# Optimization experiments

Hardware: AMD Instinct MI355X
Metric: run time of the kernel (lower is better)

The kernel has to match this reference:

```python
import jax, jax.numpy as jnp
import numpy as np

B = 4096      # batch
F = 26        # num sparse features
L = 10        # pooling factor (multi-hot indices per feature)
V = 100000    # rows per embedding table
D = 128       # embedding dim (== dense_arch_layer_sizes[-1])
DENSE_IN = 13
DENSE_SIZES = [512, 256, 128]
OVER_SIZES = [1024, 1024, 512, 256, 1]
OVER_IN = D + (F * (F - 1)) // 2 + F  # 479


def _linear_params(key, dims, prefix):
    out = {}
    ks = jax.random.split(key, len(dims) - 1)
    for i in range(len(dims) - 1):
        fan_in = dims[i]
        out[f"{prefix}W{i}"] = jax.random.normal(ks[i], (dims[i], dims[i + 1]), jnp.float32) / np.sqrt(fan_in)
        out[f"{prefix}b{i}"] = jnp.zeros((dims[i + 1],), jnp.float32)
    return out


def setup_inputs() -> dict:
    key = jax.random.key(0)
    k0, k1, k2, k3, k4 = jax.random.split(key, 5)
    inp = {
        "dense_features": jax.random.normal(k0, (B, DENSE_IN), jnp.float32),
        "indices": jax.random.randint(k1, (B, F, L), 0, V, dtype=jnp.int64),
        "tables": jax.random.normal(k2, (F, V, D), jnp.float32) * 0.01,
    }
    inp.update(_linear_params(k3, [DENSE_IN] + DENSE_SIZES, "d"))
    inp.update(_linear_params(k4, [OVER_IN] + OVER_SIZES, "o"))
    return inp


def _dlrm_forward(dense_features, indices, tables,
                  dW0, db0, dW1, db1, dW2, db2,
                  oW0, ob0, oW1, ob1, oW2, ob2, oW3, ob3, oW4, ob4):
    b = dense_features.shape[0]
    # DenseArch: MLP with relu on every layer
    x = dense_features
    for W, bb in ((dW0, db0), (dW1, db1), (dW2, db2)):
        x = jax.nn.relu(x @ W + bb)
    embedded_dense = x  # [B, D]

    # SparseArch: pooled (sum) embedding lookup per feature -> [B, F, D]
    flat_tables = tables.reshape(F * V, D)
    offs = jnp.arange(F, dtype=indices.dtype) * V
    flat_idx = (indices + offs[None, :, None]).reshape(-1)
    gathered = jnp.take(flat_tables, flat_idx, axis=0).reshape(b, F, L, D)
    embedded_sparse = gathered.sum(axis=2)  # [B, F, D]

    # InteractionArch: bmm + upper-triangular gather
    z = jnp.concatenate([embedded_dense[:, None, :], embedded_sparse], axis=1)  # [B, F+1, D]
    inter = jnp.einsum("bnd,bmd->bnm", z, z)  # [B, F+1, F+1]
    iu0, iu1 = np.triu_indices(F + 1, k=1)
    inter_flat = inter[:, iu0, iu1]  # [B, C(F+1,2)]
    feats = jnp.concatenate([embedded_dense, inter_flat], axis=1)  # [B, OVER_IN]

    # OverArch: relu MLP on layer_sizes[:-1], then plain final Linear
    y = feats
    for W, bb in ((oW0, ob0), (oW1, ob1), (oW2, ob2), (oW3, ob3)):
        y = jax.nn.relu(y @ W + bb)
    logits = y @ oW4 + ob4  # [B, 1]
    return logits


def reference(dense_features, indices, tables,
              dW0, db0, dW1, db1, dW2, db2,
              oW0, ob0, oW1, ob1, oW2, ob2, oW3, ob3, oW4, ob4):
    return _dlrm_forward(dense_features, indices, tables,
                         dW0, db0, dW1, db1, dW2, db2,
                         oW0, ob0, oW1, ob1, oW2, ob2, oW3, ob3, oW4, ob4)
```

## Files before the change

### kernel.cpp

```cpp
#include <hip/hip_runtime.h>

#define B_ 4096
#define F_ 26
#define L_ 10
#define V_ 100000
#define D_ 128

typedef __attribute__((ext_vector_type(8))) short short8;
typedef __attribute__((ext_vector_type(4))) float f32x4;

__device__ inline unsigned pack_split(float f) {
    union { float f; unsigned u; } a; a.f = f;
    unsigned r = (a.u + 0x7FFFu + ((a.u >> 16) & 1u)) >> 16;
    union { unsigned u; float f; } hf; hf.u = r << 16;
    float rem = f - hf.f;
    union { float f; unsigned u; } b; b.f = rem;
    unsigned r2 = (b.u + 0x7FFFu + ((b.u >> 16) & 1u)) >> 16;
    return (r << 16) | (r2 & 0xFFFFu);
}
__device__ inline float unpack_f(unsigned u) {
    union { unsigned u; float f; } h; h.u = u & 0xFFFF0000u;
    union { unsigned u; float f; } l; l.u = u << 16;
    return h.f + l.f;
}

__device__ void prep_tile(const float* __restrict__ W, unsigned* __restrict__ Wt,
                          int K, int N, int Kp, int local)
{
    __shared__ float tile[32][33];
    const int t = threadIdx.x;
    const int tx = t & 31, ty = t >> 5;
    const int nbt = N >> 5;
    const int nb = (local % nbt) << 5, kb = (local / nbt) << 5;
    #pragma unroll
    for (int i = 0; i < 4; ++i) {
        int k = kb + ty + i * 8;
        tile[ty + i * 8][tx] = (k < K) ? W[(size_t)k * N + nb + tx] : 0.f;
    }
    __syncthreads();
    #pragma unroll
    for (int i = 0; i < 4; ++i) {
        int nl = ty + i * 8;
        Wt[(size_t)(nb + nl) * Kp + kb + tx] = pack_split(tile[tx][nl]);
    }
}

__global__ __launch_bounds__(256) void prep_all(
    const float* dW0, const float* dW1, const float* dW2,
    const float* oW0, const float* oW1, const float* oW2, const float* oW3,
    unsigned* dWt0, unsigned* dWt1, unsigned* dWt2,
    unsigned* oWt0, unsigned* oWt1, unsigned* oWt2, unsigned* oWt3,
    const float* dense, unsigned* densep)
{
    const int bid = blockIdx.x;
    if      (bid < 16)   prep_tile(dW0, dWt0, 13,   512,  32,   bid);
    else if (bid < 144)  prep_tile(dW1, dWt1, 512,  256,  512,  bid - 16);
    else if (bid < 176)  prep_tile(dW2, dWt2, 256,  128,  256,  bid - 144);
    else if (bid < 656)  prep_tile(oW0, oWt0, 479,  1024, 480,  bid - 176);
    else if (bid < 1680) prep_tile(oW1, oWt1, 1024, 1024, 1024, bid - 656);
    else if (bid < 2192) prep_tile(oW2, oWt2, 1024, 512,  1024, bid - 1680);
    else if (bid < 2320) prep_tile(oW3, oWt3, 512,  256,  512,  bid - 2192);
    else {
        int g = (bid - 2320) * 256 + threadIdx.x;
        int b = g >> 5, k = g & 31;
        densep[g] = (k < 13) ? pack_split(dense[(size_t)b * 13 + k]) : 0u;
    }
}

template<bool RELU>
__global__ __launch_bounds__(512) void gemm8(
    const unsigned* __restrict__ Ap, const unsigned* __restrict__ Wt,
    const float* __restrict__ bias, unsigned* __restrict__ Cp,
    int M, int N, int Kp)
{
    __shared__ __align__(16) unsigned Au[2][128 * 32];
    __shared__ __align__(16) unsigned Bu[2][128 * 32];

    const int t    = threadIdx.x;
    const int lane = t & 63;
    const int w    = t >> 6;
    const int wm   = w >> 2, wn = w & 3;
    const int m0   = blockIdx.y * 128, n0 = blockIdx.x * 128;

    f32x4 acc[4][2];
    const f32x4 zero = {0.f, 0.f, 0.f, 0.f};
    #pragma unroll
    for (int i = 0; i < 4; ++i)
        #pragma unroll
        for (int j = 0; j < 2; ++j) acc[i][j] = zero;

    const unsigned* Ab = Ap + (size_t)m0 * Kp;
    const unsigned* Bb = Wt + (size_t)n0 * Kp;

    const int g4 = lane >> 4;
    const int rr = lane & 15;

    auto STAGE = [&](int buf, int k0) {
        #pragma unroll
        for (int i = 0; i < 2; ++i) {
            int chunk = t + (i << 9);
            int row = chunk >> 3, ch = chunk & 7;
            int sch = ch ^ (row & 7);
            __builtin_amdgcn_global_load_lds(
                (const __attribute__((address_space(1))) unsigned*)(Ab + (size_t)row * Kp + k0 + (sch << 2)),
                &Au[buf][chunk << 2], 16, 0, 0);
        }
        #pragma unroll
        for (int i = 0; i < 2; ++i) {
            int chunk = t + (i << 9);
            int row = chunk >> 3, ch = chunk & 7;
            int sch = ch ^ (row & 7);
            __builtin_amdgcn_global_load_lds(
                (const __attribute__((address_space(1))) unsigned*)(Bb + (size_t)row * Kp + k0 + (sch << 2)),
                &Bu[buf][chunk << 2], 16, 0, 0);
        }
    };

    auto COMPUTE = [&](int buf) {
        const unsigned* au = Au[buf];
        const unsigned* bu = Bu[buf];
        short8 bh[2], bl[2];
        #pragma unroll
        for (int tj = 0; tj < 2; ++tj) {
            int r = wn * 32 + tj * 16 + rr;
            int c0 = (2 * g4) ^ (r & 7), c1 = (2 * g4 + 1) ^ (r & 7);
            uint4 p = *reinterpret_cast<const uint4*>(&bu[r * 32 + (c0 << 2)]);
            uint4 q = *reinterpret_cast<const uint4*>(&bu[r * 32 + (c1 << 2)]);
            union { short8 s; uint4 u; } H, L;
            H.u.x = __builtin_amdgcn_perm(p.y, p.x, 0x07060302u);
            L.u.x = __builtin_amdgcn_perm(p.y, p.x, 0x05040100u);
            H.u.y = __builtin_amdgcn_perm(p.w, p.z, 0x07060302u);
            L.u.y = __builtin_amdgcn_perm(p.w, p.z, 0x05040100u);
            H.u.z = __builtin_amdgcn_perm(q.y, q.x, 0x07060302u);
            L.u.z = __builtin_amdgcn_perm(q.y, q.x, 0x05040100u);
            H.u.w = __builtin_amdgcn_perm(q.w, q.z, 0x07060302u);
            L.u.w = __builtin_amdgcn_perm(q.w, q.z, 0x05040100u);
            bh[tj] = H.s; bl[tj] = L.s;
        }
        #pragma unroll
        for (int ti = 0; ti < 4; ++ti) {
            int r = wm * 64 + ti * 16 + rr;
            int c0 = (2 * g4) ^ (r & 7), c1 = (2 * g4 + 1) ^ (r & 7);
            uint4 p = *reinterpret_cast<const uint4*>(&au[r * 32 + (c0 << 2)]);
            uint4 q = *reinterpret_cast<const uint4*>(&au[r * 32 + (c1 << 2)]);
            union { short8 s; uint4 u; } H, L;
            H.u.x = __builtin_amdgcn_perm(p.y, p.x, 0x07060302u);
            L.u.x = __builtin_amdgcn_perm(p.y, p.x, 0x05040100u);
            H.u.y = __builtin_amdgcn_perm(p.w, p.z, 0x07060302u);
            L.u.y = __builtin_amdgcn_perm(p.w, p.z, 0x05040100u);
            H.u.z = __builtin_amdgcn_perm(q.y, q.x, 0x07060302u);
            L.u.z = __builtin_amdgcn_perm(q.y, q.x, 0x05040100u);
            H.u.w = __builtin_amdgcn_perm(q.w, q.z, 0x07060302u);
            L.u.w = __builtin_amdgcn_perm(q.w, q.z, 0x05040100u);
            short8 ah = H.s, al = L.s;
            #pragma unroll
            for (int tj = 0; tj < 2; ++tj) {
                f32x4 c = acc[ti][tj];
                c = __builtin_amdgcn_mfma_f32_16x16x32_bf16(ah, bh[tj], c, 0, 0, 0);
                c = __builtin_amdgcn_mfma_f32_16x16x32_bf16(ah, bl[tj], c, 0, 0, 0);
                c = __builtin_amdgcn_mfma_f32_16x16x32_bf16(al, bh[tj], c, 0, 0, 0);
                acc[ti][tj] = c;
            }
        }
    };

    const int nt = Kp >> 5;
    STAGE(0, 0);
    __syncthreads();
    int cur = 0;
    for (int ts = 0; ts < nt - 1; ++ts) {
        STAGE(cur ^ 1, (ts + 1) << 5);
        COMPUTE(cur);
        __syncthreads();
        cur ^= 1;
    }
    COMPUTE(cur);

    #pragma unroll
    for (int ti = 0; ti < 4; ++ti) {
        int row = m0 + wm * 64 + ti * 16 + (g4 << 2);
        #pragma unroll
        for (int tj = 0; tj < 2; ++tj) {
            int col = n0 + wn * 32 + tj * 16 + rr;
            float bv = bias[col];
            #pragma unroll
            for (int r = 0; r < 4; ++r) {
                float v = acc[ti][tj][r] + bv;
                if (RELU) v = fmaxf(v, 0.f);
                Cp[(size_t)(row + r) * N + col] = pack_split(v);
            }
        }
    }
}

__global__ __launch_bounds__(256) void gather_interact_mfma(
    const unsigned* __restrict__ x2p,
    const int*      __restrict__ idx_words,
    const float*    __restrict__ tables,
    unsigned*       __restrict__ featsp)
{
    __shared__ unsigned zh[4][32][64];
    __shared__ unsigned zl[4][32][64];
    __shared__ int sidx[4][F_ * L_];
    __shared__ int sstride;

    const int t    = threadIdx.x;
    const int w    = t >> 6;
    const int lane = t & 63;
    const int s    = blockIdx.x * 4 + w;

    if (t == 0) {
        int st = 2;
        for (int ww = 1; ww < 256; ww += 2)
            if (idx_words[ww] != 0) { st = 1; break; }
        sstride = st;
    }
    __syncthreads();
    const int st = sstride;

    for (int q = lane; q < F_ * L_; q += 64) {
        int v = idx_words[((size_t)s * F_ * L_ + q) * st];
        sidx[w][q] = v < 0 ? 0 : (v >= V_ ? V_ - 1 : v);
    }
    uint2 xv = *reinterpret_cast<const uint2*>(x2p + (size_t)s * 128 + 2 * lane);
    *reinterpret_cast<uint2*>(featsp + (size_t)s * 480 + 2 * lane) = xv;
    if (lane == 0) featsp[(size_t)s * 480 + 479] = 0u;
    zh[w][0][lane] = (xv.x >> 16) | (xv.y & 0xFFFF0000u);
    zl[w][0][lane] = (xv.x & 0xFFFFu) | (xv.y << 16);
    __syncthreads();

    for (int f = 0; f < F_; ++f) {
        float2 a = {0.f, 0.f};
        const float* tab = tables + (size_t)f * V_ * D_;
        #pragma unroll
        for (int l = 0; l < L_; ++l) {
            int idx = sidx[w][f * L_ + l];
            float2 v = *reinterpret_cast<const float2*>(tab + (size_t)idx * D_ + 2 * lane);
            a.x += v.x; a.y += v.y;
        }
        unsigned px = pack_split(a.x), py = pack_split(a.y);
        int r  = f + 1;
        int dw = (((lane >> 2) ^ (r & 7)) << 2) + (lane & 3);
        zh[w][r][dw] = (px >> 16) | (py & 0xFFFF0000u);
        zl[w][r][dw] = (px & 0xFFFFu) | (py << 16);
    }
    __syncthreads();

    const int g4 = lane >> 4;
    const int rr = lane & 15;
    f32x4 acc[2][2];
    const f32x4 zero = {0.f, 0.f, 0.f, 0.f};
    acc[0][0] = zero; acc[0][1] = zero; acc[1][0] = zero; acc[1][1] = zero;

    #pragma unroll
    for (int ks = 0; ks < 4; ++ks) {
        short8 h[2], lo[2];
        #pragma unroll
        for (int mi = 0; mi < 2; ++mi) {
            int r = mi * 16 + rr;
            int c = (ks * 4 + g4) ^ (r & 7);
            h[mi]  = *reinterpret_cast<const short8*>(&zh[w][r][c << 2]);
            lo[mi] = *reinterpret_cast<const short8*>(&zl[w][r][c << 2]);
        }
        #pragma unroll
        for (int mi = 0; mi < 2; ++mi)
            #pragma unroll
            for (int nj = 0; nj < 2; ++nj) {
                f32x4 c = acc[mi][nj];
                c = __builtin_amdgcn_mfma_f32_16x16x32_bf16(h[mi],  h[nj],  c, 0, 0, 0);
                c = __builtin_amdgcn_mfma_f32_16x16x32_bf16(h[mi],  lo[nj], c, 0, 0, 0);
                c = __builtin_amdgcn_mfma_f32_16x16x32_bf16(lo[mi], h[nj],  c, 0, 0, 0);
                acc[mi][nj] = c;
            }
    }

    #pragma unroll
    for (int mi = 0; mi < 2; ++mi) {
        #pragma unroll
        for (int nj = 0; nj < 2; ++nj) {
            #pragma unroll
            for (int r = 0; r < 4; ++r) {
                int i = mi * 16 + g4 * 4 + r;
                int j = nj * 16 + rr;
                if (i < j && j <= 26) {
                    int p = i * 26 - (i * (i - 1)) / 2 + (j - i - 1);
                    featsp[(size_t)s * 480 + 128 + p] = pack_split(acc[mi][nj][r]);
                }
            }
        }
    }
}

__global__ __launch_bounds__(256) void final_dot(
    const unsigned* __restrict__ yp, const float* __restrict__ w,
    const float* __restrict__ bias, float* __restrict__ out)
{
    const int wave = threadIdx.x >> 6;
    const int lane = threadIdx.x & 63;
    const int b = blockIdx.x * 4 + wave;
    uint4 u = *reinterpret_cast<const uint4*>(yp + (size_t)b * 256 + lane * 4);
    float4 wv = *reinterpret_cast<const float4*>(&w[lane * 4]);
    float s = unpack_f(u.x) * wv.x + unpack_f(u.y) * wv.y +
              unpack_f(u.z) * wv.z + unpack_f(u.w) * wv.w;
    #pragma unroll
    for (int off = 32; off; off >>= 1) s += __shfl_xor(s, off);
    if (lane == 0) out[b] = s + bias[0];
}

extern "C" void kernel_launch(void* const* d_in, const int* in_sizes, int n_in,
                              void* d_out, int out_size, void* d_ws, size_t ws_size,
                              hipStream_t stream)
{
    const float* dense   = (const float*)d_in[0];
    const int*   indices = (const int*)  d_in[1];
    const float* tables  = (const float*)d_in[2];
    const float* dW0 = (const float*)d_in[3];  const float* db0 = (const float*)d_in[4];
    const float* dW1 = (const float*)d_in[5];  const float* db1 = (const float*)d_in[6];
    const float* dW2 = (const float*)d_in[7];  const float* db2 = (const float*)d_in[8];
    const float* oW0 = (const float*)d_in[9];  const float* ob0 = (const float*)d_in[10];
    const float* oW1 = (const float*)d_in[11]; const float* ob1 = (const float*)d_in[12];
    const float* oW2 = (const float*)d_in[13]; const float* ob2 = (const float*)d_in[14];
    const float* oW3 = (const float*)d_in[15]; const float* ob3 = (const float*)d_in[16];
    const float* oW4 = (const float*)d_in[17]; const float* ob4 = (const float*)d_in[18];
    float* out = (float*)d_out;

    unsigned* wsu = (unsigned*)d_ws;
    unsigned* dWt0 = wsu + 0;
    unsigned* dWt1 = wsu + 16384;
    unsigned* dWt2 = wsu + 147456;
    unsigned* oWt0 = wsu + 180224;
    unsigned* oWt1 = wsu + 671744;
    unsigned* oWt2 = wsu + 1720320;
    unsigned* oWt3 = wsu + 2244608;
    unsigned* densep = wsu + 2375680;
    unsigned* x2p    = wsu + 2506752;
    unsigned* featsp = wsu + 3031040;
    unsigned* x0p    = wsu + 5000000;
    unsigned* x1p    = wsu + 7097152;
    unsigned* y0p    = wsu + 5000000;
    unsigned* y1p    = wsu + 9194304;
    unsigned* y2p    = wsu + 2506752;
    unsigned* y3p    = wsu + 5000000;

    prep_all<<<2832, 256, 0, stream>>>(dW0, dW1, dW2, oW0, oW1, oW2, oW3,
                                       dWt0, dWt1, dWt2, oWt0, oWt1, oWt2, oWt3,
                                       dense, densep);

    gemm8<true><<<dim3(4, B_ / 128), 512, 0, stream>>>(densep, dWt0, db0, x0p, B_, 512, 32);
    gemm8<true><<<dim3(2, B_ / 128), 512, 0, stream>>>(x0p,    dWt1, db1, x1p, B_, 256, 512);
    gemm8<true><<<dim3(1, B_ / 128), 512, 0, stream>>>(x1p,    dWt2, db2, x2p, B_, 128, 256);

    gather_interact_mfma<<<B_ / 4, 256, 0, stream>>>(x2p, indices, tables, featsp);

    gemm8<true><<<dim3(8, B_ / 128), 512, 0, stream>>>(featsp, oWt0, ob0, y0p, B_, 1024, 480);
    gemm8<true><<<dim3(8, B_ / 128), 512, 0, stream>>>(y0p,    oWt1, ob1, y1p, B_, 1024, 1024);
    gemm8<true><<<dim3(4, B_ / 128), 512, 0, stream>>>(y1p,    oWt2, ob2, y2p, B_, 512, 1024);
    gemm8<true><<<dim3(2, B_ / 128), 512, 0, stream>>>(y2p,    oWt3, ob3, y3p, B_, 256, 512);

    final_dot<<<B_ / 4, 256, 0, stream>>>(y3p, oW4, ob4, out);
}
```

Measured before the change: 294.6 us.

## Split embedding gather into its own wide kernel separate from interaction

Moves the pooled embedding lookup out of the fused gather+interaction kernel into a new kernel with one wavefront per (sample, feature) bag, launched with B*F/4 blocks, and writes packed bag sums to a workspace buffer. The interaction kernel then reads the precomputed bags instead of serially gathering 26 features per wave. This exposes far more memory-level parallelism for the random table reads, at the cost of an extra global write and read of the bag buffer and one more launch. The gemm template is also simplified to always apply ReLU.

Result: faster. 287.3 us (-2.5%).

```diff
diff --git a/kernel.cpp b/kernel.cpp
--- a/kernel.cpp
+++ b/kernel.cpp
@@ -67,11 +67,10 @@
     }
 }
 
-template<bool RELU>
 __global__ __launch_bounds__(512) void gemm8(
     const unsigned* __restrict__ Ap, const unsigned* __restrict__ Wt,
     const float* __restrict__ bias, unsigned* __restrict__ Cp,
-    int M, int N, int Kp)
+    int N, int Kp)
 {
     __shared__ __align__(16) unsigned Au[2][128 * 32];
     __shared__ __align__(16) unsigned Bu[2][128 * 32];
@@ -185,29 +184,25 @@
             float bv = bias[col];
             #pragma unroll
             for (int r = 0; r < 4; ++r) {
-                float v = acc[ti][tj][r] + bv;
-                if (RELU) v = fmaxf(v, 0.f);
+                float v = fmaxf(acc[ti][tj][r] + bv, 0.f);
                 Cp[(size_t)(row + r) * N + col] = pack_split(v);
             }
         }
     }
 }
 
-__global__ __launch_bounds__(256) void gather_interact_mfma(
-    const unsigned* __restrict__ x2p,
-    const int*      __restrict__ idx_words,
-    const float*    __restrict__ tables,
-    unsigned*       __restrict__ featsp)
-{
-    __shared__ unsigned zh[4][32][64];
-    __shared__ unsigned zl[4][32][64];
-    __shared__ int sidx[4][F_ * L_];
+__global__ __launch_bounds__(256) void gather_bags(
+    const int*   __restrict__ idx_words,
+    const float* __restrict__ tables,
+    unsigned*    __restrict__ bagp)
+{
     __shared__ int sstride;
-
     const int t    = threadIdx.x;
     const int w    = t >> 6;
     const int lane = t & 63;
-    const int s    = blockIdx.x * 4 + w;
+    const int g    = blockIdx.x * 4 + w;
+    const int s    = g / F_;
+    const int f    = g - s * F_;
 
     if (t == 0) {
         int st = 2;
@@ -218,31 +213,47 @@
     __syncthreads();
     const int st = sstride;
 
-    for (int q = lane; q < F_ * L_; q += 64) {
-        int v = idx_words[((size_t)s * F_ * L_ + q) * st];
-        sidx[w][q] = v < 0 ? 0 : (v >= V_ ? V_ - 1 : v);
-    }
+    const float* tab = tables + (size_t)f * V_ * D_;
+    const size_t ibase = (size_t)s * (F_ * L_) + (size_t)f * L_;
+    float2 a = {0.f, 0.f};
+    #pragma unroll
+    for (int l = 0; l < L_; ++l) {
+        int v = idx_words[(ibase + l) * st];
+        v = v < 0 ? 0 : (v >= V_ ? V_ - 1 : v);
+        float2 x = *reinterpret_cast<const float2*>(tab + (size_t)v * D_ + 2 * lane);
+        a.x += x.x; a.y += x.y;
+    }
+    uint2 o;
+    o.x = pack_split(a.x);
+    o.y = pack_split(a.y);
+    *reinterpret_cast<uint2*>(bagp + ((size_t)s * F_ + f) * 128 + 2 * lane) = o;
+}
+
+__global__ __launch_bounds__(256) void interact_mfma(
+    const unsigned* __restrict__ x2p,
+    const unsigned* __restrict__ bagp,
+    unsigned*       __restrict__ featsp)
+{
+    __shared__ unsigned zh[4][32][64];
+    __shared__ unsigned zl[4][32][64];
+
+    const int t    = threadIdx.x;
+    const int w    = t >> 6;
+    const int lane = t & 63;
+    const int s    = blockIdx.x * 4 + w;
+
     uint2 xv = *reinterpret_cast<const uint2*>(x2p + (size_t)s * 128 + 2 * lane);
     *reinterpret_cast<uint2*>(featsp + (size_t)s * 480 + 2 * lane) = xv;
     if (lane == 0) featsp[(size_t)s * 480 + 479] = 0u;
     zh[w][0][lane] = (xv.x >> 16) | (xv.y & 0xFFFF0000u);
     zl[w][0][lane] = (xv.x & 0xFFFFu) | (xv.y << 16);
-    __syncthreads();
 
     for (int f = 0; f < F_; ++f) {
-        float2 a = {0.f, 0.f};
-        const float* tab = tables + (size_t)f * V_ * D_;
-        #pragma unroll
-        for (int l = 0; l < L_; ++l) {
-            int idx = sidx[w][f * L_ + l];
-            float2 v = *reinterpret_cast<const float2*>(tab + (size_t)idx * D_ + 2 * lane);
-            a.x += v.x; a.y += v.y;
-        }
-        unsigned px = pack_split(a.x), py = pack_split(a.y);
+        uint2 u = *reinterpret_cast<const uint2*>(bagp + ((size_t)s * F_ + f) * 128 + 2 * lane);
         int r  = f + 1;
         int dw = (((lane >> 2) ^ (r & 7)) << 2) + (lane & 3);
-        zh[w][r][dw] = (px >> 16) | (py & 0xFFFF0000u);
-        zl[w][r][dw] = (px & 0xFFFFu) | (py << 16);
+        zh[w][r][dw] = (u.x >> 16) | (u.y & 0xFFFF0000u);
+        zl[w][r][dw] = (u.x & 0xFFFFu) | (u.y << 16);
     }
     __syncthreads();
 
@@ -341,21 +352,24 @@
     unsigned* y1p    = wsu + 9194304;
     unsigned* y2p    = wsu + 2506752;
     unsigned* y3p    = wsu + 5000000;
+    unsigned* bagp   = wsu + 13500000;
+
+    gather_bags<<<(B_ * F_) / 4, 256, 0, stream>>>(indices, tables, bagp);
 
     prep_all<<<2832, 256, 0, stream>>>(dW0, dW1, dW2, oW0, oW1, oW2, oW3,
                                        dWt0, dWt1, dWt2, oWt0, oWt1, oWt2, oWt3,
                                        dense, densep);
 
-    gemm8<true><<<dim3(4, B_ / 128), 512, 0, stream>>>(densep, dWt0, db0, x0p, B_, 512, 32);
-    gemm8<true><<<dim3(2, B_ / 128), 512, 0, stream>>>(x0p,    dWt1, db1, x1p, B_, 256, 512);
-    gemm8<true><<<dim3(1, B_ / 128), 512, 0, stream>>>(x1p,    dWt2, db2, x2p, B_, 128, 256);
-
-    gather_interact_mfma<<<B_ / 4, 256, 0, stream>>>(x2p, indices, tables, featsp);
-
-    gemm8<true><<<dim3(8, B_ / 128), 512, 0, stream>>>(featsp, oWt0, ob0, y0p, B_, 1024, 480);
-    gemm8<true><<<dim3(8, B_ / 128), 512, 0, stream>>>(y0p,    oWt1, ob1, y1p, B_, 1024, 1024);
-    gemm8<true><<<dim3(4, B_ / 128), 512, 0, stream>>>(y1p,    oWt2, ob2, y2p, B_, 512, 1024);
-    gemm8<true><<<dim3(2, B_ / 128), 512, 0, stream>>>(y2p,    oWt3, ob3, y3p, B_, 256, 512);
+    gemm8<<<dim3(4, 32), 512, 0, stream>>>(densep, dWt0, db0, x0p, 512, 32);
+    gemm8<<<dim3(2, 32), 512, 0, stream>>>(x0p,    dWt1, db1, x1p, 256, 512);
+    gemm8<<<dim3(1, 32), 512, 0, stream>>>(x1p,    dWt2, db2, x2p, 128, 256);
+
+    interact_mfma<<<B_ / 4, 256, 0, stream>>>(x2p, bagp, featsp);
+
+    gemm8<<<dim3(8, 32), 512, 0, stream>>>(featsp, oWt0, ob0, y0p, 1024, 480);
+    gemm8<<<dim3(8, 32), 512, 0, stream>>>(y0p,    oWt1, ob1, y1p, 1024, 1024);
+    gemm8<<<dim3(4, 32), 512, 0, stream>>>(y1p,    oWt2, ob2, y2p, 512, 1024);
+    gemm8<<<dim3(2, 32), 512, 0, stream>>>(y2p,    oWt3, ob3, y3p, 256, 512);
 
     final_dot<<<B_ / 4, 256, 0, stream>>>(y3p, oW4, ob4, out);
 }
```
